# Kernel optimization log

Measured on AMD Instinct MI355X. Metric: run time of the kernel, lower is better.

The kernel has to match this reference:

```python
import jax, jax.numpy as jnp
import numpy as np

INPUT_DIM = 1024
EMBED_DIM = 1024
NUM_HEADS = 16
HEAD_DIM = EMBED_DIM // NUM_HEADS


def setup_inputs() -> dict:
    key = jax.random.key(0)
    k_x, k_qkv, k_w, k_b = jax.random.split(key, 4)
    B, N = 2, 2048
    x = jax.random.normal(k_x, (B, N, INPUT_DIM), dtype=jnp.float32)
    # nn.Linear weights: stored [out, in]; scale like torch default init
    s1 = 1.0 / np.sqrt(INPUT_DIM)
    s2 = 1.0 / np.sqrt(EMBED_DIM)
    W_qkv = jax.random.uniform(k_qkv, (3 * EMBED_DIM, INPUT_DIM), jnp.float32, -s1, s1)
    W_out = jax.random.uniform(k_w, (EMBED_DIM, EMBED_DIM), jnp.float32, -s2, s2)
    b_out = jax.random.uniform(k_b, (EMBED_DIM,), jnp.float32, -s2, s2)
    return {"x": x, "W_qkv": W_qkv, "W_out": W_out, "b_out": b_out}


def reference(x, W_qkv, W_out, b_out):
    B, N, C = x.shape
    # qkv projection (no bias): [B, N, 3*embed]
    qkv = jnp.einsum('bnc,ec->bne', x, W_qkv)
    q = qkv[:, :, 0:EMBED_DIM].reshape(B, N, NUM_HEADS, HEAD_DIM)
    k = qkv[:, :, EMBED_DIM:2 * EMBED_DIM].reshape(B, N, NUM_HEADS, HEAD_DIM)
    v = qkv[:, :, 2 * EMBED_DIM:3 * EMBED_DIM].reshape(B, N, NUM_HEADS, HEAD_DIM)
    scores = jnp.einsum('bihd,bjhd->bhij', q, k) / jnp.sqrt(jnp.float32(HEAD_DIM))
    attn = jax.nn.softmax(scores, axis=-1)
    out = jnp.einsum('bhij,bjhd->bihd', attn, v).reshape(B, N, EMBED_DIM)
    return jnp.einsum('bne,oe->bno', out, W_out) + b_out
```

## Files before the change

### kernel.cpp

```cpp
#include <hip/hip_runtime.h>
#include <stdint.h>

typedef __attribute__((ext_vector_type(8))) short short8;
typedef __attribute__((ext_vector_type(4))) short bf16x4;
typedef __attribute__((ext_vector_type(4))) float f32x4;

#define MFMA32(a, b, c) __builtin_amdgcn_mfma_f32_16x16x32_bf16((a), (b), (c), 0, 0, 0)
#define MFMA16(a, b, c) __builtin_amdgcn_mfma_f32_16x16x16bf16_1k((a), (b), (c), 0, 0, 0)

__device__ __forceinline__ uint16_t f32_to_bf16(float f) {
  union { float f; uint32_t u; } v; v.f = f;
  uint32_t u = v.u;
  u += 0x7FFFu + ((u >> 16) & 1u);
  return (uint16_t)(u >> 16);
}
__device__ __forceinline__ uint16_t f32_to_bf16_fast(float f) {
  union { float f; uint32_t u; } v; v.f = f;
  return (uint16_t)((v.u + 0x8000u) >> 16);
}

__device__ __forceinline__ void load_lds16(const uint16_t* g, uint16_t* l) {
  __builtin_amdgcn_global_load_lds(
      (const __attribute__((address_space(1))) uint32_t*)g,
      (__attribute__((address_space(3))) uint32_t*)l, 16, 0, 0);
}

__global__ __launch_bounds__(256) void cvt3_kernel(
    const float* __restrict__ x, const float* __restrict__ w1,
    const float* __restrict__ w2, uint16_t* __restrict__ xb,
    uint16_t* __restrict__ w1b, uint16_t* __restrict__ w2b) {
  const int i = blockIdx.x * 256 + threadIdx.x;
  const float4* src;
  ushort4* dst;
  int off;
  if (i < 1048576) { src = (const float4*)x;  dst = (ushort4*)xb;  off = i; }
  else if (i < 1835008) { src = (const float4*)w1; dst = (ushort4*)w1b; off = i - 1048576; }
  else { src = (const float4*)w2; dst = (ushort4*)w2b; off = i - 1835008; }
  const float4 v = src[off];
  ushort4 o;
  o.x = f32_to_bf16(v.x);
  o.y = f32_to_bf16(v.y);
  o.z = f32_to_bf16(v.z);
  o.w = f32_to_bf16(v.w);
  dst[off] = o;
}

__global__ __launch_bounds__(256) void gemm_qkv_kernel(
    const uint16_t* __restrict__ A, const uint16_t* __restrict__ Bt,
    uint16_t* __restrict__ Qh, uint16_t* __restrict__ Kh, uint16_t* __restrict__ Vh) {
  __shared__ __align__(16) uint16_t As[128 * 64];
  __shared__ __align__(16) uint16_t Bs[128 * 64];
  const int tid = threadIdx.x;
  const int wave = tid >> 6;
  const int lane = tid & 63;
  const int quad = lane >> 4;
  const int l16 = lane & 15;
  const int row0 = blockIdx.x * 128;
  const int col0 = blockIdx.y * 128;
  const int wm = (wave >> 1) * 64;
  const int wn = (wave & 1) * 64;
  const int K = 1024;

  f32x4 acc[4][4];
#pragma unroll
  for (int a = 0; a < 4; ++a)
#pragma unroll
    for (int b = 0; b < 4; ++b) acc[a][b] = (f32x4){0.f, 0.f, 0.f, 0.f};

  const int swz8 = ((lane & 7) ^ ((lane >> 3) & 7)) * 8;
  const uint16_t* gA = A + (size_t)(row0 + wave * 32 + (lane >> 3)) * K + swz8;
  const uint16_t* gB = Bt + (size_t)(col0 + wave * 32 + (lane >> 3)) * K + swz8;

  for (int k0 = 0; k0 < K; k0 += 64) {
#pragma unroll
    for (int s = 0; s < 4; ++s) {
      load_lds16(gA + (size_t)s * 8 * K + k0, &As[(wave * 32 + s * 8) * 64]);
      load_lds16(gB + (size_t)s * 8 * K + k0, &Bs[(wave * 32 + s * 8) * 64]);
    }
    __syncthreads();
#pragma unroll
    for (int ks = 0; ks < 2; ++ks) {
      const int cswz = (((ks * 4 + quad) ^ (l16 & 7)) * 8);
      short8 af[4], bf[4];
#pragma unroll
      for (int mt = 0; mt < 4; ++mt)
        af[mt] = *(const short8*)&As[(wm + mt * 16 + l16) * 64 + cswz];
#pragma unroll
      for (int nt = 0; nt < 4; ++nt)
        bf[nt] = *(const short8*)&Bs[(wn + nt * 16 + l16) * 64 + cswz];
#pragma unroll
      for (int mt = 0; mt < 4; ++mt)
#pragma unroll
        for (int nt = 0; nt < 4; ++nt)
          acc[mt][nt] = MFMA32(af[mt], bf[nt], acc[mt][nt]);
    }
    __syncthreads();
  }

#pragma unroll
  for (int mt = 0; mt < 4; ++mt) {
#pragma unroll
    for (int nt = 0; nt < 4; ++nt) {
      const int col = col0 + wn + nt * 16 + l16;
      const int which = col >> 10;
      const int hc = (col & 1023) >> 6;
      const int d = col & 63;
#pragma unroll
      for (int r = 0; r < 4; ++r) {
        const int row = row0 + wm + mt * 16 + quad * 4 + r;
        const float val = acc[mt][nt][r];
        const int b = row >> 11;
        const int nn = row & 2047;
        const size_t hb = (size_t)(b * 16 + hc) * 131072;
        if (which == 0) {
          Qh[hb + (size_t)nn * 64 + d] = f32_to_bf16(val * 0.1803368801111244f);
        } else if (which == 1) {
          const uint16_t bv = f32_to_bf16(val);
          const int jt = nn >> 6, st = (nn >> 4) & 3, j16 = nn & 15;
          const int kc = d >> 5, qd = (d >> 3) & 3, e = d & 7;
          Kh[hb + jt * 4096 + st * 1024 + kc * 512 + (qd * 16 + j16) * 8 + e] = bv;
        } else {
          const uint16_t bv = f32_to_bf16(val);
          const int jt = nn >> 6, j = nn & 63;
          const int st = j >> 4, qv = (j >> 2) & 3, e = j & 3;
          const int tt = d >> 4, d16 = d & 15;
          Vh[hb + jt * 4096 + ((st * 2 + (tt >> 1)) * 64 + qv * 16 + d16) * 8 +
             (tt & 1) * 4 + e] = bv;
        }
      }
    }
  }
}

__global__ __launch_bounds__(256) void gemm_out_kernel(
    const uint16_t* __restrict__ A, const uint16_t* __restrict__ Bt,
    float* __restrict__ Cf, const float* __restrict__ bias) {
  __shared__ __align__(16) uint16_t As[128 * 64];
  __shared__ __align__(16) uint16_t Bs[64 * 64];
  const int tid = threadIdx.x;
  const int wave = tid >> 6;
  const int lane = tid & 63;
  const int quad = lane >> 4;
  const int l16 = lane & 15;
  const int row0 = blockIdx.x * 128;
  const int col0 = blockIdx.y * 64;
  const int wm = (wave >> 1) * 64;
  const int wn = (wave & 1) * 32;
  const int K = 1024;
  const int N = 1024;

  f32x4 acc[4][2];
#pragma unroll
  for (int a = 0; a < 4; ++a)
#pragma unroll
    for (int b = 0; b < 2; ++b) acc[a][b] = (f32x4){0.f, 0.f, 0.f, 0.f};

  const int swz8 = ((lane & 7) ^ ((lane >> 3) & 7)) * 8;
  const uint16_t* gA = A + (size_t)(row0 + wave * 32 + (lane >> 3)) * K + swz8;
  const uint16_t* gB = Bt + (size_t)(col0 + wave * 16 + (lane >> 3)) * K + swz8;

  for (int k0 = 0; k0 < K; k0 += 64) {
#pragma unroll
    for (int s = 0; s < 4; ++s)
      load_lds16(gA + (size_t)s * 8 * K + k0, &As[(wave * 32 + s * 8) * 64]);
#pragma unroll
    for (int s = 0; s < 2; ++s)
      load_lds16(gB + (size_t)s * 8 * K + k0, &Bs[(wave * 16 + s * 8) * 64]);
    __syncthreads();
#pragma unroll
    for (int ks = 0; ks < 2; ++ks) {
      const int cswz = (((ks * 4 + quad) ^ (l16 & 7)) * 8);
      short8 af[4], bf[2];
#pragma unroll
      for (int mt = 0; mt < 4; ++mt)
        af[mt] = *(const short8*)&As[(wm + mt * 16 + l16) * 64 + cswz];
#pragma unroll
      for (int nt = 0; nt < 2; ++nt)
        bf[nt] = *(const short8*)&Bs[(wn + nt * 16 + l16) * 64 + cswz];
#pragma unroll
      for (int mt = 0; mt < 4; ++mt)
#pragma unroll
        for (int nt = 0; nt < 2; ++nt)
          acc[mt][nt] = MFMA32(af[mt], bf[nt], acc[mt][nt]);
    }
    __syncthreads();
  }

#pragma unroll
  for (int mt = 0; mt < 4; ++mt) {
#pragma unroll
    for (int nt = 0; nt < 2; ++nt) {
      const int col = col0 + wn + nt * 16 + l16;
#pragma unroll
      for (int r = 0; r < 4; ++r) {
        const int row = row0 + wm + mt * 16 + quad * 4 + r;
        Cf[(size_t)row * N + col] = acc[mt][nt][r] + bias[col];
      }
    }
  }
}

__global__ __launch_bounds__(256, 2) void attn_kernel(
    const uint16_t* __restrict__ Qh, const uint16_t* __restrict__ Kh,
    const uint16_t* __restrict__ Vh, uint16_t* __restrict__ out) {
  __shared__ __align__(16) uint16_t Ks[2][4096];
  __shared__ __align__(16) uint16_t Vs[2][4096];
  const int tid = threadIdx.x;
  const int wave = tid >> 6;
  const int lane = tid & 63;
  const int quad = lane >> 4;
  const int l16 = lane & 15;
  const int bx = blockIdx.x;
  const int it = bx & 15;
  const int h = (bx >> 4) & 15;
  const int ib = bx >> 8;
  const int i0 = it * 128 + wave * 32;
  const size_t hb = (size_t)(ib * 16 + h) * 131072;

  short8 qf[2][2];
#pragma unroll
  for (int m = 0; m < 2; ++m)
#pragma unroll
    for (int kc = 0; kc < 2; ++kc)
      qf[m][kc] = *(const short8*)(Qh + hb + (size_t)(i0 + m * 16 + l16) * 64 + kc * 32 + quad * 8);

  f32x4 o[2][4], o4[2];
#pragma unroll
  for (int m = 0; m < 2; ++m) {
    o4[m] = (f32x4){0.f, 0.f, 0.f, 0.f};
#pragma unroll
    for (int t = 0; t < 4; ++t) o[m][t] = (f32x4){0.f, 0.f, 0.f, 0.f};
  }

  const bf16x4 ones4 = {(short)0x3F80, (short)0x3F80, (short)0x3F80, (short)0x3F80};

  const uint16_t* gK = Kh + hb + wave * 1024 + lane * 8;
  const uint16_t* gV = Vh + hb + wave * 1024 + lane * 8;
  const int so = wave * 1024;

  load_lds16(gK, &Ks[0][so]);
  load_lds16(gK + 512, &Ks[0][so + 512]);
  load_lds16(gV, &Vs[0][so]);
  load_lds16(gV + 512, &Vs[0][so + 512]);
  __syncthreads();

#pragma unroll 2
  for (int t = 0; t < 32; ++t) {
    const int cur = t & 1;
    if (t < 31) {
      const size_t goff = (size_t)(t + 1) * 4096;
      load_lds16(gK + goff, &Ks[cur ^ 1][so]);
      load_lds16(gK + goff + 512, &Ks[cur ^ 1][so + 512]);
      load_lds16(gV + goff, &Vs[cur ^ 1][so]);
      load_lds16(gV + goff + 512, &Vs[cur ^ 1][so + 512]);
    }

    short8 kf[8];
#pragma unroll
    for (int i = 0; i < 8; ++i) kf[i] = *(const short8*)&Ks[cur][i * 512 + lane * 8];

    f32x4 s[2][4];
#pragma unroll
    for (int m = 0; m < 2; ++m)
#pragma unroll
      for (int st = 0; st < 4; ++st) {
        f32x4 sc = (f32x4){0.f, 0.f, 0.f, 0.f};
        sc = MFMA32(kf[st * 2 + 0], qf[m][0], sc);
        sc = MFMA32(kf[st * 2 + 1], qf[m][1], sc);
        s[m][st] = sc;
      }

    short8 v8[8];
#pragma unroll
    for (int i = 0; i < 8; ++i) v8[i] = *(const short8*)&Vs[cur][i * 512 + lane * 8];

    bf16x4 p4[2][4];
#pragma unroll
    for (int m = 0; m < 2; ++m)
#pragma unroll
      for (int st = 0; st < 4; ++st) {
        bf16x4 p;
#pragma unroll
        for (int r = 0; r < 4; ++r)
          p[r] = (short)f32_to_bf16_fast(__builtin_amdgcn_exp2f(s[m][st][r]));
        p4[m][st] = p;
      }

#pragma unroll
    for (int st = 0; st < 4; ++st) {
#pragma unroll
      for (int m = 0; m < 2; ++m) {
        o4[m] = MFMA16(p4[m][st], ones4, o4[m]);
#pragma unroll
        for (int tth = 0; tth < 2; ++tth) {
          const short8 w = v8[st * 2 + tth];
          const bf16x4 vlo = {w[0], w[1], w[2], w[3]};
          const bf16x4 vhi = {w[4], w[5], w[6], w[7]};
          o[m][tth * 2 + 0] = MFMA16(p4[m][st], vlo, o[m][tth * 2 + 0]);
          o[m][tth * 2 + 1] = MFMA16(p4[m][st], vhi, o[m][tth * 2 + 1]);
        }
      }
    }

    __syncthreads();
  }

#pragma unroll
  for (int m = 0; m < 2; ++m)
#pragma unroll
    for (int r = 0; r < 4; ++r) {
      const float inv = 1.0f / o4[m][r];
      const int row = i0 + m * 16 + quad * 4 + r;
      const size_t obase = (size_t)(ib * 2048 + row) * 1024 + h * 64;
#pragma unroll
      for (int tt = 0; tt < 4; ++tt)
        out[obase + tt * 16 + l16] = f32_to_bf16(o[m][tt][r] * inv);
    }
}

extern "C" void kernel_launch(void* const* d_in, const int* in_sizes, int n_in,
                              void* d_out, int out_size, void* d_ws, size_t ws_size,
                              hipStream_t stream) {
  const float* x = (const float*)d_in[0];
  const float* Wqkv = (const float*)d_in[1];
  const float* Wout = (const float*)d_in[2];
  const float* bout = (const float*)d_in[3];

  uint16_t* xb = (uint16_t*)d_ws;
  uint16_t* wqkvb = xb + (size_t)4096 * 1024;
  uint16_t* woutb = wqkvb + (size_t)3072 * 1024;
  uint16_t* qh = woutb + (size_t)1024 * 1024;
  uint16_t* kh = qh + (size_t)32 * 131072;
  uint16_t* vh = kh + (size_t)32 * 131072;
  uint16_t* attnb = vh + (size_t)32 * 131072;

  cvt3_kernel<<<8192, 256, 0, stream>>>(x, Wqkv, Wout, xb, wqkvb, woutb);

  gemm_qkv_kernel<<<dim3(4096 / 128, 3072 / 128), 256, 0, stream>>>(
      xb, wqkvb, qh, kh, vh);

  attn_kernel<<<512, 256, 0, stream>>>(qh, kh, vh, attnb);

  gemm_out_kernel<<<dim3(4096 / 128, 1024 / 64), 256, 0, stream>>>(
      attnb, woutb, (float*)d_out, bout);
}
```

Before: 185.0 us.

## Halve attention query tile per wave, double grid, and map heads to XCDs

Each wave now processes 16 query rows instead of 32, so the attention grid doubles to 1024 blocks and launch bounds allow 4 blocks per CU. Block indices are remapped so that each XCD handles a fixed subset of heads, aiming to keep K/V for a head resident in one XCD's L2. This raises occupancy and latency hiding but halves the reuse of each K/V tile loaded into LDS, doubling K/V load traffic per query.

New measurement: 186.2 us. About the same (+0.7%).

```diff
diff --git a/kernel.cpp b/kernel.cpp
--- a/kernel.cpp
+++ b/kernel.cpp
@@ -200,7 +200,7 @@
   }
 }
 
-__global__ __launch_bounds__(256, 2) void attn_kernel(
+__global__ __launch_bounds__(256, 4) void attn_kernel(
     const uint16_t* __restrict__ Qh, const uint16_t* __restrict__ Kh,
     const uint16_t* __restrict__ Vh, uint16_t* __restrict__ out) {
   __shared__ __align__(16) uint16_t Ks[2][4096];
@@ -211,26 +211,23 @@
   const int quad = lane >> 4;
   const int l16 = lane & 15;
   const int bx = blockIdx.x;
-  const int it = bx & 15;
-  const int h = (bx >> 4) & 15;
-  const int ib = bx >> 8;
-  const int i0 = it * 128 + wave * 32;
+  const int xcd = bx & 7;
+  const int g = bx >> 3;
+  const int it = g & 31;
+  const int h = ((g >> 5) & 1) * 8 + xcd;
+  const int ib = g >> 6;
+  const int i0 = it * 64 + wave * 16;
   const size_t hb = (size_t)(ib * 16 + h) * 131072;
 
-  short8 qf[2][2];
-#pragma unroll
-  for (int m = 0; m < 2; ++m)
-#pragma unroll
-    for (int kc = 0; kc < 2; ++kc)
-      qf[m][kc] = *(const short8*)(Qh + hb + (size_t)(i0 + m * 16 + l16) * 64 + kc * 32 + quad * 8);
-
-  f32x4 o[2][4], o4[2];
-#pragma unroll
-  for (int m = 0; m < 2; ++m) {
-    o4[m] = (f32x4){0.f, 0.f, 0.f, 0.f};
-#pragma unroll
-    for (int t = 0; t < 4; ++t) o[m][t] = (f32x4){0.f, 0.f, 0.f, 0.f};
-  }
+  short8 qf[2];
+#pragma unroll
+  for (int kc = 0; kc < 2; ++kc)
+    qf[kc] = *(const short8*)(Qh + hb + (size_t)(i0 + l16) * 64 + kc * 32 + quad * 8);
+
+  f32x4 o[4], o4;
+  o4 = (f32x4){0.f, 0.f, 0.f, 0.f};
+#pragma unroll
+  for (int t = 0; t < 4; ++t) o[t] = (f32x4){0.f, 0.f, 0.f, 0.f};
 
   const bf16x4 ones4 = {(short)0x3F80, (short)0x3F80, (short)0x3F80, (short)0x3F80};
 
@@ -259,63 +256,54 @@
 #pragma unroll
     for (int i = 0; i < 8; ++i) kf[i] = *(const short8*)&Ks[cur][i * 512 + lane * 8];
 
-    f32x4 s[2][4];
-#pragma unroll
-    for (int m = 0; m < 2; ++m)
-#pragma unroll
-      for (int st = 0; st < 4; ++st) {
-        f32x4 sc = (f32x4){0.f, 0.f, 0.f, 0.f};
-        sc = MFMA32(kf[st * 2 + 0], qf[m][0], sc);
-        sc = MFMA32(kf[st * 2 + 1], qf[m][1], sc);
-        s[m][st] = sc;
+    f32x4 s[4];
+#pragma unroll
+    for (int st = 0; st < 4; ++st) {
+      f32x4 sc = (f32x4){0.f, 0.f, 0.f, 0.f};
+      sc = MFMA32(kf[st * 2 + 0], qf[0], sc);
+      sc = MFMA32(kf[st * 2 + 1], qf[1], sc);
+      s[st] = sc;
+    }
+
+    short8 v8[8];
+#pragma unroll
+    for (int i = 0; i < 8; ++i) v8[i] = *(const short8*)&Vs[cur][i * 512 + lane * 8];
+
+    bf16x4 p4[4];
+#pragma unroll
+    for (int st = 0; st < 4; ++st) {
+      bf16x4 p;
+#pragma unroll
+      for (int r = 0; r < 4; ++r)
+        p[r] = (short)f32_to_bf16_fast(__builtin_amdgcn_exp2f(s[st][r]));
+      p4[st] = p;
+    }
+
+#pragma unroll
+    for (int st = 0; st < 4; ++st) {
+      o4 = MFMA16(p4[st], ones4, o4);
+#pragma unroll
+      for (int tth = 0; tth < 2; ++tth) {
+        const short8 w = v8[st * 2 + tth];
+        const bf16x4 vlo = {w[0], w[1], w[2], w[3]};
+        const bf16x4 vhi = {w[4], w[5], w[6], w[7]};
+        o[tth * 2 + 0] = MFMA16(p4[st], vlo, o[tth * 2 + 0]);
+        o[tth * 2 + 1] = MFMA16(p4[st], vhi, o[tth * 2 + 1]);
       }
-
-    short8 v8[8];
-#pragma unroll
-    for (int i = 0; i < 8; ++i) v8[i] = *(const short8*)&Vs[cur][i * 512 + lane * 8];
-
-    bf16x4 p4[2][4];
-#pragma unroll
-    for (int m = 0; m < 2; ++m)
-#pragma unroll
-      for (int st = 0; st < 4; ++st) {
-        bf16x4 p;
-#pragma unroll
-        for (int r = 0; r < 4; ++r)
-          p[r] = (short)f32_to_bf16_fast(__builtin_amdgcn_exp2f(s[m][st][r]));
-        p4[m][st] = p;
-      }
-
-#pragma unroll
-    for (int st = 0; st < 4; ++st) {
-#pragma unroll
-      for (int m = 0; m < 2; ++m) {
-        o4[m] = MFMA16(p4[m][st], ones4, o4[m]);
-#pragma unroll
-        for (int tth = 0; tth < 2; ++tth) {
-          const short8 w = v8[st * 2 + tth];
-          const bf16x4 vlo = {w[0], w[1], w[2], w[3]};
-          const bf16x4 vhi = {w[4], w[5], w[6], w[7]};
-          o[m][tth * 2 + 0] = MFMA16(p4[m][st], vlo, o[m][tth * 2 + 0]);
-          o[m][tth * 2 + 1] = MFMA16(p4[m][st], vhi, o[m][tth * 2 + 1]);
-        }
-      }
-    }
-
-    __syncthreads();
-  }
-
-#pragma unroll
-  for (int m = 0; m < 2; ++m)
-#pragma unroll
-    for (int r = 0; r < 4; ++r) {
-      const float inv = 1.0f / o4[m][r];
-      const int row = i0 + m * 16 + quad * 4 + r;
-      const size_t obase = (size_t)(ib * 2048 + row) * 1024 + h * 64;
-#pragma unroll
-      for (int tt = 0; tt < 4; ++tt)
-        out[obase + tt * 16 + l16] = f32_to_bf16(o[m][tt][r] * inv);
-    }
+    }
+
+    __syncthreads();
+  }
+
+#pragma unroll
+  for (int r = 0; r < 4; ++r) {
+    const float inv = 1.0f / o4[r];
+    const int row = i0 + quad * 4 + r;
+    const size_t obase = (size_t)(ib * 2048 + row) * 1024 + h * 64;
+#pragma unroll
+    for (int tt = 0; tt < 4; ++tt)
+      out[obase + tt * 16 + l16] = f32_to_bf16(o[tt][r] * inv);
+  }
 }
 
 extern "C" void kernel_launch(void* const* d_in, const int* in_sizes, int n_in,
@@ -339,7 +327,7 @@
   gemm_qkv_kernel<<<dim3(4096 / 128, 3072 / 128), 256, 0, stream>>>(
       xb, wqkvb, qh, kh, vh);
 
-  attn_kernel<<<512, 256, 0, stream>>>(qh, kh, vh, attnb);
+  attn_kernel<<<1024, 256, 0, stream>>>(qh, kh, vh, attnb);
 
   gemm_out_kernel<<<dim3(4096 / 128, 1024 / 64), 256, 0, stream>>>(
       attnb, woutb, (float*)d_out, bout);
```
